# Kernel optimization log

Hardware: AMD Instinct MI355X
Metric: run time of the kernel (lower is better)

The kernel has to match this reference:

```python
import jax, jax.numpy as jnp
import numpy as np

IN_C, OUT_C, K = 32, 32, 3
PAD = 1


def setup_inputs() -> dict:
    key = jax.random.key(0)
    kx, kw, kb = jax.random.split(key, 3)
    x = jax.random.normal(kx, (16, IN_C, 256, 256), dtype=jnp.float32)
    # Kaiming-ish init scale for the conv weight, matching nn.Conv2d defaults roughly
    fan_in = IN_C * K * K
    w = jax.random.normal(kw, (OUT_C, IN_C, K, K), dtype=jnp.float32) / np.sqrt(fan_in)
    b = jax.random.normal(kb, (OUT_C,), dtype=jnp.float32) * 0.01
    return {"x": x, "weight": w, "bias": b}


def reference(x, weight, bias):
    # Faithful math of SparseConv2d.forward: the block-sparse Triton path computes
    # the same result as a dense conv (zero blocks contribute zero), so the
    # reference is a standard 3x3 stride-1 pad-1 conv, NCHW / OIHW layout.
    y = jax.lax.conv_general_dilated(
        x, weight,
        window_strides=(1, 1),
        padding=((PAD, PAD), (PAD, PAD)),
        dimension_numbers=("NCHW", "OIHW", "NCHW"),
    )
    return y + bias[None, :, None, None]
```

## Files before the change

kernel.cpp:

```cpp
#include <hip/hip_runtime.h>


constexpr int N_  = 16;
constexpr int C_  = 32;
constexpr int OC_ = 32;
constexpr int H_  = 256;
constexpr int W_  = 256;

constexpr int XSTR = 20;
constexpr int XROW = 258 * XSTR;
constexpr int WSTRD = 36;
constexpr int WELEMS = 9 * 32 * WSTRD;
constexpr int WBYTES = WELEMS * 2;

typedef __attribute__((ext_vector_type(4)))  short short4v;
typedef __attribute__((ext_vector_type(8)))  short short8v;
typedef __attribute__((ext_vector_type(16))) float float16v;

static __device__ __forceinline__ unsigned short f2bf(float f) {
    unsigned int u = __float_as_uint(f);
    unsigned int r = (u + 0x7FFFu + ((u >> 16) & 1u)) >> 16;
    return (unsigned short)r;
}

static __device__ __forceinline__ unsigned cvtpk(float lo, float hi) {
    unsigned r;
    asm("v_cvt_pk_bf16_f32 %0, %1, %2" : "=v"(r) : "v"(lo), "v"(hi));
    return r;
}

static __device__ __forceinline__ short8v load8(const unsigned short* p) {
    short4v lo = *(const short4v*)p;
    short4v hi = *(const short4v*)(p + 4);
    return __builtin_shufflevector(lo, hi, 0, 1, 2, 3, 4, 5, 6, 7);
}

__global__ void conv_w_prep(const float* __restrict__ wgt,
                            unsigned short* __restrict__ wp) {
    const int i = blockIdx.x * 256 + threadIdx.x;
    if (i >= OC_ * C_ * 9) return;
    const float v = wgt[i];
    const int oc  = i / 288;
    const int rem = i - oc * 288;
    const int ic  = rem / 9;
    const int t9  = rem - ic * 9;
    wp[(t9 * 32 + oc) * WSTRD + ic] = f2bf(v);
}

template<bool USE_WS>
__global__ __launch_bounds__(256, 3) void conv3x3_mfma_kernel(
    const float* __restrict__ x,
    const float* __restrict__ wgt,
    const float* __restrict__ bias,
    const unsigned short* __restrict__ wpk,
    float* __restrict__ out)
{
    __shared__ __align__(16) unsigned short ldsX[3 * XROW];
    __shared__ __align__(16) unsigned short ldsW[WELEMS];

    const int tid = threadIdx.x;

    const int id = blockIdx.x;
    const int L  = (id & 7) * 512 + (id >> 3);
    const int n  = L >> 8;
    const int h  = L & (H_ - 1);

    const int lane = tid & 63;
    const int wv   = tid >> 6;
    const int col  = lane & 31;
    const int qd   = lane >> 5;
    const int wlo  = tid & 31;
    const int icp  = tid >> 5;
    const int w0a  = wv * 64;
    const int w0b  = wv * 64 + 32;
    const size_t HW = (size_t)H_ * W_;

    float2 pa[3][4], pb[3][4];
    auto load_half = [&](int half, float2 (&ra)[3][4], float2 (&rb)[3][4]) {
        const int icg = half * 16 + 2 * icp;
        const float* base = x + (size_t)(n * C_ + icg) * HW;
        #pragma unroll
        for (int r = 0; r < 3; ++r) {
            const int hy = h + r - 1;
            if (hy >= 0 && hy < H_) {
                const float* p0 = base + (size_t)hy * W_;
                const float* p1 = p0 + HW;
                #pragma unroll
                for (int wb = 0; wb < 4; ++wb) {
                    const int w = wb * 64 + 2 * wlo;
                    ra[r][wb] = *(const float2*)(p0 + w);
                    rb[r][wb] = *(const float2*)(p1 + w);
                }
            } else {
                #pragma unroll
                for (int wb = 0; wb < 4; ++wb) {
                    ra[r][wb] = make_float2(0.f, 0.f);
                    rb[r][wb] = make_float2(0.f, 0.f);
                }
            }
        }
    };
    load_half(0, pa, pb);

    if (USE_WS) {
        const int4* src = (const int4*)wpk;
        int4* dst = (int4*)&ldsW[0];
        #pragma unroll
        for (int i2 = 0; i2 < 6; ++i2) {
            const int idx = tid + i2 * 256;
            if (idx < WBYTES / 16) dst[idx] = src[idx];
        }
    } else {
        for (int i = tid; i < OC_ * C_ * 9; i += 256) {
            const float v = wgt[i];
            const int oc  = i / 288;
            const int rem = i - oc * 288;
            const int ic  = rem / 9;
            const int t9  = rem - ic * 9;
            ldsW[(t9 * 32 + oc) * WSTRD + ic] = f2bf(v);
        }
    }

    float16v acc0, acc1;
    #pragma unroll
    for (int r = 0; r < 16; ++r) {
        const float bv = bias[(r & 3) + 8 * (r >> 2) + 4 * qd];
        acc0[r] = bv;
        acc1[r] = bv;
    }

    auto write_half = [&](float2 (&ra)[3][4], float2 (&rb)[3][4]) {
        #pragma unroll
        for (int r = 0; r < 3; ++r) {
            unsigned short* dst = &ldsX[r * XROW];
            #pragma unroll
            for (int wb = 0; wb < 4; ++wb) {
                const int w = wb * 64 + 2 * wlo;
                *(unsigned*)&dst[(w + 1) * XSTR + 2 * icp] = cvtpk(ra[r][wb].x, rb[r][wb].x);
                *(unsigned*)&dst[(w + 2) * XSTR + 2 * icp] = cvtpk(ra[r][wb].y, rb[r][wb].y);
            }
        }
    };

    auto mfma_half = [&](int half) {
        #pragma unroll
        for (int kh = 0; kh < 3; ++kh) {
            #pragma unroll
            for (int kw = 0; kw < 3; ++kw) {
                const int t9 = kh * 3 + kw;
                const short8v av =
                    load8(&ldsW[(t9 * 32 + col) * WSTRD + half * 16 + qd * 8]);
                const short8v b0 =
                    load8(&ldsX[kh * XROW + (w0a + col + kw) * XSTR + qd * 8]);
                const short8v b1 =
                    load8(&ldsX[kh * XROW + (w0b + col + kw) * XSTR + qd * 8]);
                acc0 = __builtin_amdgcn_mfma_f32_32x32x16_bf16(av, b0, acc0, 0, 0, 0);
                acc1 = __builtin_amdgcn_mfma_f32_32x32x16_bf16(av, b1, acc1, 0, 0, 0);
            }
        }
    };

    write_half(pa, pb);
    if (tid < 24) {
        const int r  = tid >> 3;
        const int q  = tid & 7;
        const int wi = (q & 4) ? 257 : 0;
        const int c  = q & 3;
        *(unsigned long long*)&ldsX[r * XROW + wi * XSTR + c * 4] = 0ull;
    }
    __syncthreads();

    load_half(1, pa, pb);
    mfma_half(0);
    __syncthreads();

    write_half(pa, pb);
    __syncthreads();
    mfma_half(1);

    float* outp = out + (size_t)n * OC_ * HW + (size_t)h * W_;
    #pragma unroll
    for (int r = 0; r < 16; ++r) {
        const int oc = (r & 3) + 8 * (r >> 2) + 4 * qd;
        __builtin_nontemporal_store(acc0[r], &outp[(size_t)oc * HW + w0a + col]);
        __builtin_nontemporal_store(acc1[r], &outp[(size_t)oc * HW + w0b + col]);
    }
}

extern "C" void kernel_launch(void* const* d_in, const int* in_sizes, int n_in,
                              void* d_out, int out_size, void* d_ws, size_t ws_size,
                              hipStream_t stream) {
    const float* x    = (const float*)d_in[0];
    const float* wgt  = (const float*)d_in[1];
    const float* bias = (const float*)d_in[2];
    float* out        = (float*)d_out;

    dim3 grid(N_ * H_);
    dim3 block(256);

    if (d_ws != nullptr && ws_size >= (size_t)WBYTES) {
        unsigned short* wp = (unsigned short*)d_ws;
        conv_w_prep<<<dim3(36), dim3(256), 0, stream>>>(wgt, wp);
        conv3x3_mfma_kernel<true><<<grid, block, 0, stream>>>(x, wgt, bias, wp, out);
    } else {
        conv3x3_mfma_kernel<false><<<grid, block, 0, stream>>>(x, wgt, bias, nullptr, out);
    }
}
```

Measured before the change: 245.1 us.

## Compute two output rows per block to share input halo rows

Each block now covers two output rows with 512 threads. It stages four input rows in LDS instead of three, so the overlapping rows are shared, and it loads the weight tile once per two rows. This is meant to reduce redundant global reads of x, from three rows per output row to two, and to halve the per-block cost of staging weights. In exchange LDS use per block grows, and the launch-bounds change may limit occupancy or push registers.

```diff
diff --git a/kernel.cpp b/kernel.cpp
--- a/kernel.cpp
+++ b/kernel.cpp
@@ -48,70 +48,74 @@
 }
 
 template<bool USE_WS>
-__global__ __launch_bounds__(256, 3) void conv3x3_mfma_kernel(
+__global__ __launch_bounds__(512, 4) void conv3x3_mfma_kernel(
     const float* __restrict__ x,
     const float* __restrict__ wgt,
     const float* __restrict__ bias,
     const unsigned short* __restrict__ wpk,
     float* __restrict__ out)
 {
-    __shared__ __align__(16) unsigned short ldsX[3 * XROW];
+    __shared__ __align__(16) unsigned short ldsX[4 * XROW];
     __shared__ __align__(16) unsigned short ldsW[WELEMS];
 
     const int tid = threadIdx.x;
 
     const int id = blockIdx.x;
-    const int L  = (id & 7) * 512 + (id >> 3);
-    const int n  = L >> 8;
-    const int h  = L & (H_ - 1);
+    const int L  = (id & 7) * 256 + (id >> 3);
+    const int n  = L >> 7;
+    const int h  = (L & 127) * 2;
 
     const int lane = tid & 63;
     const int wv   = tid >> 6;
+    const int rsel = wv >> 2;
     const int col  = lane & 31;
     const int qd   = lane >> 5;
-    const int wlo  = tid & 31;
-    const int icp  = tid >> 5;
-    const int w0a  = wv * 64;
-    const int w0b  = wv * 64 + 32;
+    const int w0a  = (wv & 3) * 64;
+    const int w0b  = (wv & 3) * 64 + 32;
+
+    const int r4  = tid >> 7;
+    const int t7  = tid & 127;
+    const int wlo = t7 & 31;
+    const int icq = t7 >> 5;
     const size_t HW = (size_t)H_ * W_;
 
-    float2 pa[3][4], pb[3][4];
-    auto load_half = [&](int half, float2 (&ra)[3][4], float2 (&rb)[3][4]) {
-        const int icg = half * 16 + 2 * icp;
-        const float* base = x + (size_t)(n * C_ + icg) * HW;
-        #pragma unroll
-        for (int r = 0; r < 3; ++r) {
-            const int hy = h + r - 1;
-            if (hy >= 0 && hy < H_) {
-                const float* p0 = base + (size_t)hy * W_;
-                const float* p1 = p0 + HW;
-                #pragma unroll
-                for (int wb = 0; wb < 4; ++wb) {
-                    const int w = wb * 64 + 2 * wlo;
-                    ra[r][wb] = *(const float2*)(p0 + w);
-                    rb[r][wb] = *(const float2*)(p1 + w);
-                }
-            } else {
-                #pragma unroll
-                for (int wb = 0; wb < 4; ++wb) {
-                    ra[r][wb] = make_float2(0.f, 0.f);
-                    rb[r][wb] = make_float2(0.f, 0.f);
-                }
+    float2 a0[4], a1[4], b0r[4], b1r[4];
+    auto load_half = [&](int half) {
+        const int icg0 = half * 16 + 2 * icq;
+        const int icg1 = half * 16 + 2 * (icq + 4);
+        const int hy = h - 1 + r4;
+        if (hy >= 0 && hy < H_) {
+            const float* pA0 = x + ((size_t)(n * C_ + icg0) * H_ + hy) * W_;
+            const float* pA1 = pA0 + HW;
+            const float* pB0 = x + ((size_t)(n * C_ + icg1) * H_ + hy) * W_;
+            const float* pB1 = pB0 + HW;
+            #pragma unroll
+            for (int wb = 0; wb < 4; ++wb) {
+                const int w = wb * 64 + 2 * wlo;
+                a0[wb]  = *(const float2*)(pA0 + w);
+                a1[wb]  = *(const float2*)(pA1 + w);
+                b0r[wb] = *(const float2*)(pB0 + w);
+                b1r[wb] = *(const float2*)(pB1 + w);
             }
+        } else {
+            #pragma unroll
+            for (int wb = 0; wb < 4; ++wb) {
+                a0[wb] = a1[wb] = b0r[wb] = b1r[wb] = make_float2(0.f, 0.f);
+            }
         }
     };
-    load_half(0, pa, pb);
+    load_half(0);
 
     if (USE_WS) {
         const int4* src = (const int4*)wpk;
-        int4* dst = (int4*)&ldsW[0];
+        int4* dstW = (int4*)&ldsW[0];
         #pragma unroll
-        for (int i2 = 0; i2 < 6; ++i2) {
-            const int idx = tid + i2 * 256;
-            if (idx < WBYTES / 16) dst[idx] = src[idx];
+        for (int i2 = 0; i2 < 3; ++i2) {
+            const int idx = tid + i2 * 512;
+            if (idx < WBYTES / 16) dstW[idx] = src[idx];
         }
     } else {
-        for (int i = tid; i < OC_ * C_ * 9; i += 256) {
+        for (int i = tid; i < OC_ * C_ * 9; i += 512) {
             const float v = wgt[i];
             const int oc  = i / 288;
             const int rem = i - oc * 288;
@@ -129,16 +133,15 @@
         acc1[r] = bv;
     }
 
-    auto write_half = [&](float2 (&ra)[3][4], float2 (&rb)[3][4]) {
+    auto write_half = [&]() {
+        unsigned short* dst = &ldsX[r4 * XROW];
         #pragma unroll
-        for (int r = 0; r < 3; ++r) {
-            unsigned short* dst = &ldsX[r * XROW];
-            #pragma unroll
-            for (int wb = 0; wb < 4; ++wb) {
-                const int w = wb * 64 + 2 * wlo;
-                *(unsigned*)&dst[(w + 1) * XSTR + 2 * icp] = cvtpk(ra[r][wb].x, rb[r][wb].x);
-                *(unsigned*)&dst[(w + 2) * XSTR + 2 * icp] = cvtpk(ra[r][wb].y, rb[r][wb].y);
-            }
+        for (int wb = 0; wb < 4; ++wb) {
+            const int w = wb * 64 + 2 * wlo;
+            *(unsigned*)&dst[(w + 1) * XSTR + 2 * icq]       = cvtpk(a0[wb].x,  a1[wb].x);
+            *(unsigned*)&dst[(w + 2) * XSTR + 2 * icq]       = cvtpk(a0[wb].y,  a1[wb].y);
+            *(unsigned*)&dst[(w + 1) * XSTR + 2 * (icq + 4)] = cvtpk(b0r[wb].x, b1r[wb].x);
+            *(unsigned*)&dst[(w + 2) * XSTR + 2 * (icq + 4)] = cvtpk(b0r[wb].y, b1r[wb].y);
         }
     };
 
@@ -150,18 +153,18 @@
                 const int t9 = kh * 3 + kw;
                 const short8v av =
                     load8(&ldsW[(t9 * 32 + col) * WSTRD + half * 16 + qd * 8]);
-                const short8v b0 =
-                    load8(&ldsX[kh * XROW + (w0a + col + kw) * XSTR + qd * 8]);
-                const short8v b1 =
-                    load8(&ldsX[kh * XROW + (w0b + col + kw) * XSTR + qd * 8]);
-                acc0 = __builtin_amdgcn_mfma_f32_32x32x16_bf16(av, b0, acc0, 0, 0, 0);
-                acc1 = __builtin_amdgcn_mfma_f32_32x32x16_bf16(av, b1, acc1, 0, 0, 0);
+                const short8v bf0 =
+                    load8(&ldsX[(rsel + kh) * XROW + (w0a + col + kw) * XSTR + qd * 8]);
+                const short8v bf1 =
+                    load8(&ldsX[(rsel + kh) * XROW + (w0b + col + kw) * XSTR + qd * 8]);
+                acc0 = __builtin_amdgcn_mfma_f32_32x32x16_bf16(av, bf0, acc0, 0, 0, 0);
+                acc1 = __builtin_amdgcn_mfma_f32_32x32x16_bf16(av, bf1, acc1, 0, 0, 0);
             }
         }
     };
 
-    write_half(pa, pb);
-    if (tid < 24) {
+    write_half();
+    if (tid < 32) {
         const int r  = tid >> 3;
         const int q  = tid & 7;
         const int wi = (q & 4) ? 257 : 0;
@@ -170,15 +173,15 @@
     }
     __syncthreads();
 
-    load_half(1, pa, pb);
+    load_half(1);
     mfma_half(0);
     __syncthreads();
 
-    write_half(pa, pb);
+    write_half();
     __syncthreads();
     mfma_half(1);
 
-    float* outp = out + (size_t)n * OC_ * HW + (size_t)h * W_;
+    float* outp = out + (size_t)n * OC_ * HW + (size_t)(h + rsel) * W_;
     #pragma unroll
     for (int r = 0; r < 16; ++r) {
         const int oc = (r & 3) + 8 * (r >> 2) + 4 * qd;
@@ -195,8 +198,8 @@
     const float* bias = (const float*)d_in[2];
     float* out        = (float*)d_out;
 
-    dim3 grid(N_ * H_);
-    dim3 block(256);
+    dim3 grid(N_ * H_ / 2);
+    dim3 block(512);
 
     if (d_ws != nullptr && ws_size >= (size_t)WBYTES) {
         unsigned short* wp = (unsigned short*)d_ws;
```

New measurement: 243.3 us. Within noise of the previous version (-0.7%).
